# Performance work log

Measured on AMD Instinct MI355X. Metric: run time of the kernel, lower is better.

Reference implementation:

```python
import jax, jax.numpy as jnp
import numpy as np

D_MODEL = 256
N_LEVELS = 4
N_HEADS = 8
N_POINTS = 4
OFF_DIM = 32
D_HEAD = D_MODEL // N_HEADS
SHAPES = [(64, 64), (32, 32), (16, 16), (8, 8)]  # (H_l, W_l)
LEN_IN = sum(h * w for h, w in SHAPES)  # 5440
N_BATCH = 4
LEN_Q = LEN_IN


def _offset_bias_init():
    # replicates _reset_parameters grid_init for sampling_offsets_bias
    thetas = np.arange(N_HEADS, dtype=np.float32) * (2.0 * np.pi / N_HEADS)
    grid = np.stack([np.cos(thetas), np.sin(thetas)], -1)
    grid = grid / np.abs(grid).max(-1, keepdims=True)
    grid = np.tile(grid[:, None, None, :], (1, N_LEVELS, N_POINTS, 1))
    grid = grid * np.arange(1, N_POINTS + 1, dtype=np.float32)[None, None, :, None]
    return jnp.asarray(grid, jnp.float32)  # (H, L, K, 2)


def setup_inputs() -> dict:
    key = jax.random.key(0)
    ks = jax.random.split(key, 12)
    s = 0.02
    return {
        "query": jax.random.normal(ks[0], (N_BATCH, LEN_Q, D_MODEL), jnp.float32),
        "reference_points": jax.random.uniform(ks[1], (N_BATCH, LEN_Q, N_LEVELS, 2), jnp.float32),
        "input_flatten": jax.random.normal(ks[2], (N_BATCH, LEN_IN, D_MODEL), jnp.float32),
        "input_spatial_shapes": jnp.asarray(SHAPES, jnp.int32),
        "offset_embeds_W": jax.random.normal(ks[3], (N_HEADS * N_LEVELS * N_POINTS * OFF_DIM, D_MODEL), jnp.float32) * s,
        "sampling_offsets_W": jax.random.normal(ks[4], (N_HEADS, N_LEVELS, N_POINTS, OFF_DIM, 2), jnp.float32) * s,
        "sampling_offsets_b": _offset_bias_init(),
        "attn_W": jax.random.normal(ks[5], (N_HEADS, N_LEVELS, N_POINTS, OFF_DIM, 1), jnp.float32) * s,
        "attn_b": jax.random.normal(ks[6], (N_HEADS, N_LEVELS, N_POINTS), jnp.float32) * s,
        "value_W": jax.random.normal(ks[7], (D_MODEL, D_MODEL), jnp.float32) * (1.0 / np.sqrt(D_MODEL)),
        "value_b": jnp.zeros((D_MODEL,), jnp.float32),
        "out_W": jax.random.normal(ks[8], (D_MODEL, D_MODEL), jnp.float32) * (1.0 / np.sqrt(D_MODEL)),
        "out_b": jnp.zeros((D_MODEL,), jnp.float32),
    }


def _bilinear(v, loc, H, W):
    # v: (N, heads, H*W, d_head); loc: (N, Lq, heads, K, 2) in [0,1] (x=width, y=height)
    # matches torch grid_sample(mode=bilinear, padding=zeros, align_corners=False)
    N, Lq, Hh, K, _ = loc.shape
    x = loc[..., 0] * W - 0.5
    y = loc[..., 1] * H - 0.5
    x0 = jnp.floor(x)
    y0 = jnp.floor(y)
    wx = (x - x0).transpose(0, 2, 1, 3).reshape(N, Hh, Lq * K)[..., None]
    wy = (y - y0).transpose(0, 2, 1, 3).reshape(N, Hh, Lq * K)[..., None]
    x0i = x0.astype(jnp.int32)
    y0i = y0.astype(jnp.int32)

    def gather(xi, yi):
        valid = (xi >= 0) & (xi < W) & (yi >= 0) & (yi < H)
        idx = jnp.clip(yi, 0, H - 1) * W + jnp.clip(xi, 0, W - 1)
        idx = idx.transpose(0, 2, 1, 3).reshape(N, Hh, Lq * K)
        g = jnp.take_along_axis(v, idx[..., None], axis=2)  # (N, heads, Lq*K, d)
        m = valid.transpose(0, 2, 1, 3).reshape(N, Hh, Lq * K)
        return g * m[..., None].astype(v.dtype)

    g00 = gather(x0i, y0i)
    g01 = gather(x0i + 1, y0i)
    g10 = gather(x0i, y0i + 1)
    g11 = gather(x0i + 1, y0i + 1)
    out = (g00 * (1 - wx) * (1 - wy) + g01 * wx * (1 - wy)
           + g10 * (1 - wx) * wy + g11 * wx * wy)
    return out.reshape(N, Hh, Lq, K, -1)  # (N, heads, Lq, K, d_head)


def _forward(query, reference_points, input_flatten,
             offset_embeds_W, sampling_offsets_W, sampling_offsets_b,
             attn_W, attn_b, value_W, value_b, out_W, out_b):
    N, Lq, _ = query.shape
    # value projection
    value = input_flatten @ value_W.T + value_b                      # (N, Lin, C)
    value = value.reshape(N, -1, N_HEADS, D_HEAD)                    # (N, Lin, H, d)

    # offset embedding + activation (offset_act_name == 'silu')
    oe = jax.nn.silu(query @ offset_embeds_W.T)                      # (N, Lq, H*L*K*off)
    oe = oe.reshape(N, Lq, N_HEADS, N_LEVELS, N_POINTS, OFF_DIM)

    offs = jnp.einsum('bqhlkd,hlkdc->bqhlkc', oe, sampling_offsets_W) + sampling_offsets_b
    aw = jnp.einsum('bqhlkd,hlkd->bqhlk', oe, attn_W[..., 0]) + attn_b
    aw = jax.nn.softmax(aw.reshape(N, Lq, N_HEADS, N_LEVELS * N_POINTS), axis=-1)
    aw = aw.reshape(N, Lq, N_HEADS, N_LEVELS, N_POINTS)

    # normalize offsets by (W_l, H_l) and add reference points (2-dim branch)
    normalizer = jnp.asarray([[w, h] for h, w in SHAPES], jnp.float32)  # (L, 2)
    loc = reference_points[:, :, None, :, None, :] + offs / normalizer[None, None, None, :, None, :]

    out = jnp.zeros((N, Lq, N_HEADS, D_HEAD), jnp.float32)
    start = 0
    for lvl, (H, W) in enumerate(SHAPES):
        v_l = value[:, start:start + H * W].transpose(0, 2, 1, 3)    # (N, heads, HW, d)
        sampled = _bilinear(v_l, loc[:, :, :, lvl], H, W)            # (N, heads, Lq, K, d)
        out = out + jnp.einsum('bhqkd,bqhk->bqhd', sampled, aw[:, :, :, lvl])
        start += H * W
    out = out.reshape(N, Lq, D_MODEL)
    return out @ out_W.T + out_b


def reference(query, reference_points, input_flatten, input_spatial_shapes,
              offset_embeds_W, sampling_offsets_W, sampling_offsets_b,
              attn_W, attn_b, value_W, value_b, out_W, out_b):
    # input_spatial_shapes matches SHAPES (static pyramid)
    return _forward(query, reference_points, input_flatten,
                    offset_embeds_W, sampling_offsets_W, sampling_offsets_b,
                    attn_W, attn_b, value_W, value_b, out_W, out_b)
```

## Files before the change

kernel.cpp:

```cpp
#include <hip/hip_runtime.h>
#include <hip/hip_bf16.h>

#define NB 4
#define LQ 5440
#define DM 256
#define NH 8
#define NL 4
#define NP 4
#define OFFD 32
#define DH 32
#define MTOT (NB * LQ)
#define OEN (NH * NL * NP * OFFD)
#define NGRP (NH * NL * NP)

typedef __attribute__((ext_vector_type(8))) short bf16x8;
typedef __attribute__((ext_vector_type(4))) float f32x4;
typedef unsigned int u32;

#define GLOAD_LDS16(gp, lp) \
    __builtin_amdgcn_global_load_lds((const __attribute__((address_space(1))) u32*)(gp), \
                                     (__attribute__((address_space(3))) u32*)(lp), 16, 0, 0)

__device__ __forceinline__ float bf2f(unsigned short u) {
    union { unsigned int i; float f; } v; v.i = ((unsigned int)u) << 16; return v.f;
}
__device__ __forceinline__ unsigned short f2bf(float x) {
    __hip_bfloat16 h = __float2bfloat16(x);
    return *(unsigned short*)&h;
}
__device__ __forceinline__ u32 pk2(float a, float b) {
    return (u32)f2bf(a) | ((u32)f2bf(b) << 16);
}
__device__ __forceinline__ float silu(float x) {
    return x / (1.0f + __expf(-x));
}

__global__ __launch_bounds__(256) void k_cvt2(
    const float* __restrict__ A, unsigned short* __restrict__ Ao,
    const float* __restrict__ B, unsigned short* __restrict__ Bo, int n4)
{
    int i = blockIdx.x * 256 + threadIdx.x;
    if (i >= n4) return;
    const float* src = blockIdx.y ? B : A;
    unsigned short* dst = blockIdx.y ? Bo : Ao;
    float4 v = *(const float4*)(src + (size_t)i * 4);
    ushort4 o;
    o.x = f2bf(v.x); o.y = f2bf(v.y); o.z = f2bf(v.z); o.w = f2bf(v.w);
    *(ushort4*)(dst + (size_t)i * 4) = o;
}
__global__ __launch_bounds__(256) void k_cvt3(
    const float* __restrict__ A, unsigned short* __restrict__ Ao, int nA4,
    const float* __restrict__ B, unsigned short* __restrict__ Bo, int nB4,
    const float* __restrict__ C, unsigned short* __restrict__ Co, int nC4)
{
    int i = blockIdx.x * 256 + threadIdx.x;
    const float* src; unsigned short* dst; int n4;
    if (blockIdx.y == 0)      { src = A; dst = Ao; n4 = nA4; }
    else if (blockIdx.y == 1) { src = B; dst = Bo; n4 = nB4; }
    else                      { src = C; dst = Co; n4 = nC4; }
    if (i >= n4) return;
    float4 v = *(const float4*)(src + (size_t)i * 4);
    ushort4 o;
    o.x = f2bf(v.x); o.y = f2bf(v.y); o.z = f2bf(v.z); o.w = f2bf(v.w);
    *(ushort4*)(dst + (size_t)i * 4) = o;
}

__global__ __launch_bounds__(256) void k_prep_r(
    const float* __restrict__ SW, const float* __restrict__ AW,
    unsigned short* __restrict__ Rb)
{
    int idx = blockIdx.x * 256 + threadIdx.x;
    int gg = idx >> 9, jo = (idx >> 5) & 15, d = idx & 31;
    float v = 0.f;
    if (jo == 0)      v = SW[(gg * 32 + d) * 2 + 0];
    else if (jo == 1) v = SW[(gg * 32 + d) * 2 + 1];
    else if (jo == 2) v = AW[gg * 32 + d];
    Rb[idx] = f2bf(v);
}

__global__ __launch_bounds__(256) void k_oe_mfma(
    const unsigned short* __restrict__ Qb,
    const unsigned short* __restrict__ Wb,
    const unsigned short* __restrict__ Rb,
    const float* __restrict__ SB,
    const float* __restrict__ AB,
    float* __restrict__ offs_out,
    float* __restrict__ aw_out)
{
    __shared__ short sA[128 * 64];
    __shared__ short sB[128 * 64];
    int tid = threadIdx.x;
    int n0 = blockIdx.x * 128;
    int m0 = blockIdx.y * 128;

    int lane = tid & 63;
    int w = tid >> 6;
    int wA = w >> 1;
    int wB = w & 1;
    int lcol = lane & 15, quad = lane >> 4;

    int srow = tid >> 3;
    int sq = (tid & 7) ^ (srow & 7);
    const short* gA = (const short*)Qb + (size_t)(m0 + srow) * 256 + sq * 8;
    const short* gB = (const short*)Wb + (size_t)(n0 + srow) * 256 + sq * 8;
    short* lA = sA + w * 512;
    short* lB = sB + w * 512;

    f32x4 acc[4][4] = {};

    const short* pq = sA + (wB * 64 + lcol) * 64;
    const short* pw = sB + (wA * 64 + lcol) * 64;
    int rx7 = lcol & 7;
    int qa0 = (quad ^ rx7) * 8;
    int qa1 = ((4 + quad) ^ rx7) * 8;

    for (int kc = 0; kc < 256; kc += 64) {
#pragma unroll
        for (int j = 0; j < 4; j++) {
            GLOAD_LDS16(gA + kc + j * 32 * 256, lA + j * 2048);
            GLOAD_LDS16(gB + kc + j * 32 * 256, lB + j * 2048);
        }
        __syncthreads();
        bf16x8 a[4][2], b[4][2];
#pragma unroll
        for (int i = 0; i < 4; i++) {
            a[i][0] = *(const bf16x8*)(pw + i * 16 * 64 + qa0);
            a[i][1] = *(const bf16x8*)(pw + i * 16 * 64 + qa1);
            b[i][0] = *(const bf16x8*)(pq + i * 16 * 64 + qa0);
            b[i][1] = *(const bf16x8*)(pq + i * 16 * 64 + qa1);
        }
#pragma unroll
        for (int kh = 0; kh < 2; kh++)
#pragma unroll
            for (int i = 0; i < 4; i++)
#pragma unroll
                for (int j = 0; j < 4; j++)
                    acc[i][j] = __builtin_amdgcn_mfma_f32_16x16x32_bf16(
                        a[i][kh], b[j][kh], acc[i][j], 0, 0, 0);
        __syncthreads();
    }

    u32 ps[4][4][2];
#pragma unroll
    for (int i = 0; i < 4; i++)
#pragma unroll
        for (int j = 0; j < 4; j++) {
            ps[i][j][0] = pk2(silu(acc[i][j][0]), silu(acc[i][j][1]));
            ps[i][j][1] = pk2(silu(acc[i][j][2]), silu(acc[i][j][3]));
        }

    int srcbase = (quad & 1) * 32 + lcol;
    bool hi = quad >= 2;
    f32x4 zero = {};
#pragma unroll
    for (int g = 0; g < 2; g++) {
        int gg = (n0 + wA * 64 + g * 32) >> 5;
        bf16x8 afrag = *(const bf16x8*)(Rb + ((size_t)(gg * 16 + lcol) * 32 + quad * 8));
        float sb0 = SB[gg * 2 + 0], sb1 = SB[gg * 2 + 1], ab = AB[gg];
#pragma unroll
        for (int j = 0; j < 4; j++) {
            union { u32 u[4]; bf16x8 v; } bf;
#pragma unroll
            for (int b = 0; b < 2; b++) {
                int s = srcbase + b * 16;
#pragma unroll
                for (int c = 0; c < 2; c++) {
                    u32 x0 = (u32)__shfl((int)ps[2 * g + 0][j][c], s);
                    u32 x1 = (u32)__shfl((int)ps[2 * g + 1][j][c], s);
                    bf.u[b * 2 + c] = hi ? x1 : x0;
                }
            }
            f32x4 d2 = __builtin_amdgcn_mfma_f32_16x16x32_bf16(afrag, bf.v, zero, 0, 0, 0);
            if (quad == 0) {
                int m = m0 + wB * 64 + j * 16 + lcol;
                size_t oi = ((size_t)m * NGRP + gg) * 2;
                offs_out[oi + 0] = d2[0] + sb0;
                offs_out[oi + 1] = d2[1] + sb1;
                aw_out[(size_t)m * NGRP + gg] = d2[2] + ab;
            }
        }
    }
}

__global__ __launch_bounds__(256) void k_value_mfma(
    const unsigned short* __restrict__ Xb,
    const unsigned short* __restrict__ Wvb,
    const float* __restrict__ bias,
    unsigned short* __restrict__ Vtb)
{
    __shared__ short sA[128 * 64];
    __shared__ short sB[128 * 64];
    int tid = threadIdx.x;
    int n0 = blockIdx.x * 128;
    int m0 = blockIdx.y * 128;
    int lane = tid & 63;
    int w = tid >> 6;
    int wm = w >> 1, wn = w & 1;
    int lcol = lane & 15, lrow = lane >> 4;

    int srow = tid >> 3;
    int sq = (tid & 7) ^ (srow & 7);
    const short* gA = (const short*)Xb + (size_t)(m0 + srow) * 256 + sq * 8;
    const short* gB = (const short*)Wvb + (size_t)(n0 + srow) * 256 + sq * 8;
    short* lA = sA + w * 512;
    short* lB = sB + w * 512;

    f32x4 acc[4][4] = {};
    const short* pa = sA + (wm * 64 + lcol) * 64;
    const short* pb = sB + (wn * 64 + lcol) * 64;
    int rx7 = lcol & 7;
    int qa0 = (lrow ^ rx7) * 8;
    int qa1 = ((4 + lrow) ^ rx7) * 8;

    for (int kc = 0; kc < 256; kc += 64) {
#pragma unroll
        for (int j = 0; j < 4; j++) {
            GLOAD_LDS16(gA + kc + j * 32 * 256, lA + j * 2048);
            GLOAD_LDS16(gB + kc + j * 32 * 256, lB + j * 2048);
        }
        __syncthreads();
        bf16x8 a[4][2], b[4][2];
#pragma unroll
        for (int i = 0; i < 4; i++) {
            a[i][0] = *(const bf16x8*)(pa + i * 16 * 64 + qa0);
            a[i][1] = *(const bf16x8*)(pa + i * 16 * 64 + qa1);
            b[i][0] = *(const bf16x8*)(pb + i * 16 * 64 + qa0);
            b[i][1] = *(const bf16x8*)(pb + i * 16 * 64 + qa1);
        }
#pragma unroll
        for (int kh = 0; kh < 2; kh++)
#pragma unroll
            for (int mi = 0; mi < 4; mi++)
#pragma unroll
                for (int ni = 0; ni < 4; ni++)
                    acc[mi][ni] = __builtin_amdgcn_mfma_f32_16x16x32_bf16(
                        a[mi][kh], b[ni][kh], acc[mi][ni], 0, 0, 0);
        __syncthreads();
    }

#pragma unroll
    for (int mi = 0; mi < 4; mi++) {
#pragma unroll
        for (int ni = 0; ni < 4; ni++) {
            int n = n0 + wn * 64 + ni * 16 + lcol;
            int h = n >> 5, d = n & 31;
            float bn = bias[n];
#pragma unroll
            for (int r = 0; r < 4; r++) {
                int m = m0 + wm * 64 + mi * 16 + lrow * 4 + r;
                int b = m / LQ, q = m - b * LQ;
                Vtb[(((size_t)b * NH + h) * LQ + q) * DH + d] = f2bf(acc[mi][ni][r] + bn);
            }
        }
    }
}

__global__ __launch_bounds__(256) void k_out_mfma(
    const unsigned short* __restrict__ Xb,
    const unsigned short* __restrict__ Wob,
    const float* __restrict__ bias,
    float* __restrict__ Out)
{
    __shared__ short sA[128 * 64];
    __shared__ short sB[128 * 64];
    int tid = threadIdx.x;
    int n0 = blockIdx.x * 128;
    int m0 = blockIdx.y * 128;
    int lane = tid & 63;
    int w = tid >> 6;
    int wm = w >> 1, wn = w & 1;
    int lcol = lane & 15, lrow = lane >> 4;

    int srow = tid >> 3;
    int sq = (tid & 7) ^ (srow & 7);
    const short* gA = (const short*)Xb + (size_t)(m0 + srow) * 256 + sq * 8;
    const short* gB = (const short*)Wob + (size_t)(n0 + srow) * 256 + sq * 8;
    short* lA = sA + w * 512;
    short* lB = sB + w * 512;

    f32x4 acc[4][4] = {};
    const short* pa = sA + (wm * 64 + lcol) * 64;
    const short* pb = sB + (wn * 64 + lcol) * 64;
    int rx7 = lcol & 7;
    int qa0 = (lrow ^ rx7) * 8;
    int qa1 = ((4 + lrow) ^ rx7) * 8;

    for (int kc = 0; kc < 256; kc += 64) {
#pragma unroll
        for (int j = 0; j < 4; j++) {
            GLOAD_LDS16(gA + kc + j * 32 * 256, lA + j * 2048);
            GLOAD_LDS16(gB + kc + j * 32 * 256, lB + j * 2048);
        }
        __syncthreads();
        bf16x8 a[4][2], b[4][2];
#pragma unroll
        for (int i = 0; i < 4; i++) {
            a[i][0] = *(const bf16x8*)(pa + i * 16 * 64 + qa0);
            a[i][1] = *(const bf16x8*)(pa + i * 16 * 64 + qa1);
            b[i][0] = *(const bf16x8*)(pb + i * 16 * 64 + qa0);
            b[i][1] = *(const bf16x8*)(pb + i * 16 * 64 + qa1);
        }
#pragma unroll
        for (int kh = 0; kh < 2; kh++)
#pragma unroll
            for (int mi = 0; mi < 4; mi++)
#pragma unroll
                for (int ni = 0; ni < 4; ni++)
                    acc[mi][ni] = __builtin_amdgcn_mfma_f32_16x16x32_bf16(
                        a[mi][kh], b[ni][kh], acc[mi][ni], 0, 0, 0);
        __syncthreads();
    }

#pragma unroll
    for (int mi = 0; mi < 4; mi++) {
#pragma unroll
        for (int ni = 0; ni < 4; ni++) {
            int n = n0 + wn * 64 + ni * 16 + lcol;
            float bn = bias[n];
#pragma unroll
            for (int r = 0; r < 4; r++) {
                int m = m0 + wm * 64 + mi * 16 + lrow * 4 + r;
                Out[(size_t)m * 256 + n] = acc[mi][ni][r] + bn;
            }
        }
    }
}

__global__ __launch_bounds__(256) void k_sample(
    const unsigned short* __restrict__ Vtb,
    const float* __restrict__ refp,
    const float* __restrict__ offs,
    const float* __restrict__ awl,
    unsigned short* __restrict__ atnb)
{
    int m = blockIdx.x;
    int tid = threadIdx.x;
    __shared__ int   s_idx[128][4];
    __shared__ float s_w[128][4];

    if (tid < 128) {
        int p = tid;
        int l = (p >> 2) & 3;
        float logit = awl[(size_t)m * 128 + p];
        float mx = logit;
#pragma unroll
        for (int off = 1; off < 16; off <<= 1) mx = fmaxf(mx, __shfl_xor(mx, off));
        float e = __expf(logit - mx);
        float s = e;
#pragma unroll
        for (int off = 1; off < 16; off <<= 1) s += __shfl_xor(s, off);
        float prob = e / s;

        float ox = offs[((size_t)m * 128 + p) * 2 + 0];
        float oy = offs[((size_t)m * 128 + p) * 2 + 1];
        float rx = refp[(size_t)m * 8 + l * 2 + 0];
        float ry = refp[(size_t)m * 8 + l * 2 + 1];
        int Wl = 64 >> l;
        int base = (l == 0) ? 0 : (l == 1) ? 4096 : (l == 2) ? 5120 : 5376;
        float fW = (float)Wl;
        float x = rx * fW + ox - 0.5f;
        float y = ry * fW + oy - 0.5f;
        float x0f = floorf(x), y0f = floorf(y);
        float wx = x - x0f, wy = y - y0f;
        int x0 = (int)x0f, y0 = (int)y0f;
        int xc0 = min(max(x0, 0), Wl - 1), xc1 = min(max(x0 + 1, 0), Wl - 1);
        int yc0 = min(max(y0, 0), Wl - 1), yc1 = min(max(y0 + 1, 0), Wl - 1);
        float vx0 = (x0 >= 0 && x0 < Wl) ? 1.f : 0.f;
        float vx1 = (x0 + 1 >= 0 && x0 + 1 < Wl) ? 1.f : 0.f;
        float vy0 = (y0 >= 0 && y0 < Wl) ? 1.f : 0.f;
        float vy1 = (y0 + 1 >= 0 && y0 + 1 < Wl) ? 1.f : 0.f;
        s_idx[p][0] = (base + yc0 * Wl + xc0) * DH;
        s_idx[p][1] = (base + yc0 * Wl + xc1) * DH;
        s_idx[p][2] = (base + yc1 * Wl + xc0) * DH;
        s_idx[p][3] = (base + yc1 * Wl + xc1) * DH;
        s_w[p][0] = prob * (1.f - wx) * (1.f - wy) * vx0 * vy0;
        s_w[p][1] = prob * wx * (1.f - wy) * vx1 * vy0;
        s_w[p][2] = prob * (1.f - wx) * wy * vx0 * vy1;
        s_w[p][3] = prob * wx * wy * vx1 * vy1;
    }
    __syncthreads();

    int h = tid >> 5, d = tid & 31;
    int b = m / LQ;
    const unsigned short* vb = Vtb + ((size_t)b * NH + h) * LQ * DH + d;
    float acc = 0.f;
#pragma unroll
    for (int p16 = 0; p16 < 16; p16++) {
        int p = h * 16 + p16;
        int4 ri = *(const int4*)s_idx[p];
        float4 wv = *(const float4*)s_w[p];
        float v00 = bf2f(vb[ri.x]);
        float v01 = bf2f(vb[ri.y]);
        float v10 = bf2f(vb[ri.z]);
        float v11 = bf2f(vb[ri.w]);
        acc += wv.x * v00 + wv.y * v01 + wv.z * v10 + wv.w * v11;
    }
    atnb[(size_t)m * 256 + tid] = f2bf(acc);
}

extern "C" void kernel_launch(void* const* d_in, const int* in_sizes, int n_in,
                              void* d_out, int out_size, void* d_ws, size_t ws_size,
                              hipStream_t stream) {
    const float* query  = (const float*)d_in[0];
    const float* refp   = (const float*)d_in[1];
    const float* inflat = (const float*)d_in[2];
    const float* We  = (const float*)d_in[4];
    const float* SW  = (const float*)d_in[5];
    const float* SB  = (const float*)d_in[6];
    const float* AWw = (const float*)d_in[7];
    const float* ABb = (const float*)d_in[8];
    const float* VW  = (const float*)d_in[9];
    const float* Vb  = (const float*)d_in[10];
    const float* OW  = (const float*)d_in[11];
    const float* Ob  = (const float*)d_in[12];
    float* out = (float*)d_out;

    float* ws = (float*)d_ws;
    unsigned short* Vtb  = (unsigned short*)ws;
    float* offs          = ws + 2785280;
    float* awl           = offs + 5570560;
    unsigned short* Qbf  = (unsigned short*)(awl + 2785280);
    unsigned short* Webf = Qbf + 5570560;
    unsigned short* Xbf  = Webf + 1048576;
    unsigned short* Wvbf = Xbf + 5570560;
    unsigned short* OWbf = Wvbf + 65536;
    unsigned short* Rbf  = OWbf + 65536;
    unsigned short* atnb = Xbf;

    k_cvt2<<<dim3(5440, 2), 256, 0, stream>>>(query, Qbf, inflat, Xbf, MTOT * 256 / 4);
    k_cvt3<<<dim3(1024, 3), 256, 0, stream>>>(We, Webf, OEN * 256 / 4,
                                              VW, Wvbf, 256 * 256 / 4,
                                              OW, OWbf, 256 * 256 / 4);
    k_prep_r<<<dim3(256), 256, 0, stream>>>(SW, AWw, Rbf);

    k_value_mfma<<<dim3(2, MTOT / 128), 256, 0, stream>>>(Xbf, Wvbf, Vb, Vtb);

    k_oe_mfma<<<dim3(OEN / 128, MTOT / 128), 256, 0, stream>>>(
        Qbf, Webf, Rbf, SB, ABb, offs, awl);

    k_sample<<<dim3(MTOT), 256, 0, stream>>>(Vtb, refp, offs, awl, atnb);

    k_out_mfma<<<dim3(2, MTOT / 128), 256, 0, stream>>>(atnb, OWbf, Ob, out);
}
```

Before: 288.5 us.

## Restructure sampling kernel: 4 queries per block, corner-parallel lanes, paired bf16 loads

The sampling kernel now handles four queries per block instead of one. All 256 threads compute softmax and bilinear indices, and each index is stored with its weight as an int2 in shared memory. In the gather phase each wave takes one query, and lanes are split across the four bilinear corners and 16 channel pairs. Each lane loads two bf16 values as one 32-bit word, and the corners are reduced with xor shuffles. Smaller changes swap the float-to-bf16 conversion for manual bit rounding and replace divides with rcp intrinsics, which changes rounding and reciprocal precision slightly.

```diff
diff --git a/kernel.cpp b/kernel.cpp
--- a/kernel.cpp
+++ b/kernel.cpp
@@ -25,14 +25,19 @@
     union { unsigned int i; float f; } v; v.i = ((unsigned int)u) << 16; return v.f;
 }
 __device__ __forceinline__ unsigned short f2bf(float x) {
-    __hip_bfloat16 h = __float2bfloat16(x);
-    return *(unsigned short*)&h;
+    u32 u = __float_as_uint(x);
+    u = u + 0x7fffu + ((u >> 16) & 1u);
+    return (unsigned short)(u >> 16);
 }
 __device__ __forceinline__ u32 pk2(float a, float b) {
-    return (u32)f2bf(a) | ((u32)f2bf(b) << 16);
+    u32 ua = __float_as_uint(a), ub = __float_as_uint(b);
+    ua = ua + 0x7fffu + ((ua >> 16) & 1u);
+    ub = ub + 0x7fffu + ((ub >> 16) & 1u);
+    return (ua >> 16) | (ub & 0xffff0000u);
 }
 __device__ __forceinline__ float silu(float x) {
-    return x / (1.0f + __expf(-x));
+    float e = __expf(-x);
+    return x * __builtin_amdgcn_rcpf(1.0f + e);
 }
 
 __global__ __launch_bounds__(256) void k_cvt2(
@@ -333,13 +338,15 @@
     const float* __restrict__ awl,
     unsigned short* __restrict__ atnb)
 {
-    int m = blockIdx.x;
     int tid = threadIdx.x;
-    __shared__ int   s_idx[128][4];
-    __shared__ float s_w[128][4];
-
-    if (tid < 128) {
-        int p = tid;
+    int m_base = blockIdx.x * 4;
+    __shared__ int2 s_iw[4][128][4];
+
+#pragma unroll
+    for (int rep = 0; rep < 2; rep++) {
+        int p = tid & 127;
+        int mloc = (tid >> 7) + rep * 2;
+        int m = m_base + mloc;
         int l = (p >> 2) & 3;
         float logit = awl[(size_t)m * 128 + p];
         float mx = logit;
@@ -349,7 +356,7 @@
         float s = e;
 #pragma unroll
         for (int off = 1; off < 16; off <<= 1) s += __shfl_xor(s, off);
-        float prob = e / s;
+        float prob = e * __builtin_amdgcn_rcpf(s);
 
         float ox = offs[((size_t)m * 128 + p) * 2 + 0];
         float oy = offs[((size_t)m * 128 + p) * 2 + 1];
@@ -366,36 +373,45 @@
         int xc0 = min(max(x0, 0), Wl - 1), xc1 = min(max(x0 + 1, 0), Wl - 1);
         int yc0 = min(max(y0, 0), Wl - 1), yc1 = min(max(y0 + 1, 0), Wl - 1);
         float vx0 = (x0 >= 0 && x0 < Wl) ? 1.f : 0.f;
-        float vx1 = (x0 + 1 >= 0 && x0 + 1 < Wl) ? 1.f : 0.f;
+        float vx1 = (x0 + 1 < Wl) ? 1.f : 0.f;
         float vy0 = (y0 >= 0 && y0 < Wl) ? 1.f : 0.f;
-        float vy1 = (y0 + 1 >= 0 && y0 + 1 < Wl) ? 1.f : 0.f;
-        s_idx[p][0] = (base + yc0 * Wl + xc0) * DH;
-        s_idx[p][1] = (base + yc0 * Wl + xc1) * DH;
-        s_idx[p][2] = (base + yc1 * Wl + xc0) * DH;
-        s_idx[p][3] = (base + yc1 * Wl + xc1) * DH;
-        s_w[p][0] = prob * (1.f - wx) * (1.f - wy) * vx0 * vy0;
-        s_w[p][1] = prob * wx * (1.f - wy) * vx1 * vy0;
-        s_w[p][2] = prob * (1.f - wx) * wy * vx0 * vy1;
-        s_w[p][3] = prob * wx * wy * vx1 * vy1;
+        float vy1 = (y0 + 1 < Wl) ? 1.f : 0.f;
+        if (x0 + 1 < 0) vx1 = 0.f;
+        if (y0 + 1 < 0) vy1 = 0.f;
+        s_iw[mloc][p][0] = make_int2((base + yc0 * Wl + xc0) * 64,
+                                     __float_as_int(prob * (1.f - wx) * (1.f - wy) * vx0 * vy0));
+        s_iw[mloc][p][1] = make_int2((base + yc0 * Wl + xc1) * 64,
+                                     __float_as_int(prob * wx * (1.f - wy) * vx1 * vy0));
+        s_iw[mloc][p][2] = make_int2((base + yc1 * Wl + xc0) * 64,
+                                     __float_as_int(prob * (1.f - wx) * wy * vx0 * vy1));
+        s_iw[mloc][p][3] = make_int2((base + yc1 * Wl + xc1) * 64,
+                                     __float_as_int(prob * wx * wy * vx1 * vy1));
     }
     __syncthreads();
 
-    int h = tid >> 5, d = tid & 31;
+    int wv = tid >> 6, lane = tid & 63;
+    int corner = lane >> 4, il = lane & 15;
+    int m = m_base + wv;
     int b = m / LQ;
-    const unsigned short* vb = Vtb + ((size_t)b * NH + h) * LQ * DH + d;
-    float acc = 0.f;
-#pragma unroll
-    for (int p16 = 0; p16 < 16; p16++) {
-        int p = h * 16 + p16;
-        int4 ri = *(const int4*)s_idx[p];
-        float4 wv = *(const float4*)s_w[p];
-        float v00 = bf2f(vb[ri.x]);
-        float v01 = bf2f(vb[ri.y]);
-        float v10 = bf2f(vb[ri.z]);
-        float v11 = bf2f(vb[ri.w]);
-        acc += wv.x * v00 + wv.y * v01 + wv.z * v10 + wv.w * v11;
-    }
-    atnb[(size_t)m * 256 + tid] = f2bf(acc);
+    const char* vB = (const char*)(Vtb + (size_t)b * NH * LQ * DH);
+#pragma unroll
+    for (int h = 0; h < 8; h++) {
+        const char* ph = vB + (size_t)h * LQ * DH * 2 + il * 4;
+        float a0 = 0.f, a1 = 0.f;
+#pragma unroll
+        for (int p16 = 0; p16 < 16; p16++) {
+            int2 iw = s_iw[wv][h * 16 + p16][corner];
+            u32 v = *(const u32*)(ph + iw.x);
+            float wgt = __int_as_float(iw.y);
+            a0 += wgt * __uint_as_float(v << 16);
+            a1 += wgt * __uint_as_float(v & 0xffff0000u);
+        }
+        a0 += __shfl_xor(a0, 16); a0 += __shfl_xor(a0, 32);
+        a1 += __shfl_xor(a1, 16); a1 += __shfl_xor(a1, 32);
+        if (corner == 0) {
+            ((u32*)atnb)[(size_t)m * 128 + h * 16 + il] = pk2(a0, a1);
+        }
+    }
 }
 
 extern "C" void kernel_launch(void* const* d_in, const int* in_sizes, int n_in,
@@ -438,7 +454,7 @@
     k_oe_mfma<<<dim3(OEN / 128, MTOT / 128), 256, 0, stream>>>(
         Qbf, Webf, Rbf, SB, ABb, offs, awl);
 
-    k_sample<<<dim3(MTOT), 256, 0, stream>>>(Vtb, refp, offs, awl, atnb);
+    k_sample<<<dim3(MTOT / 4), 256, 0, stream>>>(Vtb, refp, offs, awl, atnb);
 
     k_out_mfma<<<dim3(2, MTOT / 128), 256, 0, stream>>>(atnb, OWbf, Ob, out);
 }
```

New measurement: 260.7 us. 9.7% less time.
